# Kernel optimization log

Hardware: AMD Instinct MI355X
Metric: run time of the kernel (lower is better)

The kernel has to match this reference:

```python
import jax, jax.numpy as jnp
import numpy as np
from jax import lax

DN = ('NCHW', 'OIHW', 'NCHW')
SAME = ((1, 1), (1, 1))
VALID = ((0, 0), (0, 0))


def conv(x, w, pad):
    return lax.conv_general_dilated(x, w, (1, 1), pad, dimension_numbers=DN)


def convT(x, w, strides):
    # inverse (transposed) conv; for kernel==stride this exactly inverts the
    # non-overlapping pooling rulebook used by spconv's SparseInverseConv2d
    return lax.conv_transpose(x, w, strides, 'VALID', dimension_numbers=DN)


def maxpool(x, k):
    return lax.reduce_window(x, -jnp.inf, lax.max, (1, 1) + k, (1, 1) + k, 'VALID')


def lrelu(x):
    return jnp.where(x >= 0, x, 0.01 * x)  # F.leaky_relu default slope


def setup_inputs() -> dict:
    key = jax.random.key(0)
    ks = jax.random.split(key, 14)
    B, C, H, W = 32, 6, 500, 128
    x = jax.random.normal(ks[0], (B, C, H, W), jnp.float32)  # fully dense => all voxels active

    def p(k, shape):
        return jax.random.normal(k, shape, jnp.float32) * 0.05

    return {
        'x': x,
        'w1': p(ks[1], (8, 6, 3, 3)),      # SubMConv2d 6->8
        'w2': p(ks[2], (16, 8, 3, 3)),     # SubMConv2d 8->16
        'w3': p(ks[3], (32, 16, 3, 3)),    # SubMConv2d 16->32
        'wmu': p(ks[4], (1, 32, 1, 5)),    # SparseConv2d 32->1, kernel (1,5)
        'wlv': p(ks[5], (1, 32, 1, 5)),
        'wu0': p(ks[6], (32, 1, 1, 5)),    # SparseInverseConv2d 1->32
        'wu1': p(ks[7], (32, 32, 5, 2)),   # inverse of pool3
        'w4': p(ks[8], (16, 32, 3, 3)),
        'wu2': p(ks[9], (16, 16, 5, 2)),   # inverse of pool2
        'w5': p(ks[10], (8, 16, 3, 3)),
        'wu3': p(ks[11], (8, 8, 2, 2)),    # inverse of pool1
        'w6': p(ks[12], (6, 8, 3, 3)),
    }


def reference(x, w1, w2, w3, wmu, wlv, wu0, wu1, w4, wu2, w5, wu3, w6):
    B = x.shape[0]
    # ---- encoder ----
    h = lrelu(conv(x, w1, SAME))        # [B,8,500,128]
    h = maxpool(h, (2, 2))              # [B,8,250,64]
    h = lrelu(conv(h, w2, SAME))        # [B,16,250,64]
    h = maxpool(h, (5, 2))              # [B,16,50,32]
    h = lrelu(conv(h, w3, SAME))        # [B,32,50,32]
    h = maxpool(h, (5, 2))              # [B,32,10,16]
    mu = conv(h, wmu, VALID)            # [B,1,10,12]
    logvar = conv(h, wlv, VALID)        # [B,1,10,12]
    # ---- reparameterise ----
    eps = jax.random.normal(jax.random.key(42), mu.shape, mu.dtype)
    z = mu + eps * jnp.exp(0.5 * logvar)
    # ---- decoder ----
    d = lrelu(convT(z, wu0, (1, 1)))    # [B,32,10,16]
    d = lrelu(convT(d, wu1, (5, 2)))    # [B,32,50,32]
    d = lrelu(conv(d, w4, SAME))        # [B,16,50,32]
    d = lrelu(convT(d, wu2, (5, 2)))    # [B,16,250,64]
    d = lrelu(conv(d, w5, SAME))        # [B,8,250,64]
    d = lrelu(convT(d, wu3, (2, 2)))    # [B,8,500,128]
    d = lrelu(conv(d, w6, SAME))        # [B,6,500,128]
    return (d, mu.reshape(B, -1), logvar.reshape(B, -1), z.reshape(B, -1))
```

## Files before the change

kernel.cpp:

```cpp
#include <hip/hip_runtime.h>
#include <stdint.h>

#define DI __device__ __forceinline__

DI float lrelu(float x){ return x >= 0.0f ? x : 0.01f*x; }

DI uint32_t rotl32(uint32_t x, int d){ return (x << d) | (x >> (32 - d)); }

DI void threefry_0_42(uint32_t& x0, uint32_t& x1){
  const uint32_t ks0 = 0u, ks1 = 42u, ks2 = 0x1BD11BF0u;
  x0 += ks0; x1 += ks1;
  #define TFR(d) { x0 += x1; x1 = rotl32(x1,(d)); x1 ^= x0; }
  TFR(13) TFR(15) TFR(26) TFR(6)  x0 += ks1; x1 += ks2 + 1u;
  TFR(17) TFR(29) TFR(16) TFR(24) x0 += ks2; x1 += ks0 + 2u;
  TFR(13) TFR(15) TFR(26) TFR(6)  x0 += ks0; x1 += ks1 + 3u;
  TFR(17) TFR(29) TFR(16) TFR(24) x0 += ks1; x1 += ks2 + 4u;
  TFR(13) TFR(15) TFR(26) TFR(6)  x0 += ks2; x1 += ks0 + 5u;
  #undef TFR
}

DI float erfinv_f32(float x){
  float w = -log1pf(-x*x);
  float p;
  if (w < 5.0f){
    w = w - 2.5f;
    p = 2.81022636e-08f;
    p = fmaf(p, w, 3.43273939e-07f);
    p = fmaf(p, w, -3.5233877e-06f);
    p = fmaf(p, w, -4.39150654e-06f);
    p = fmaf(p, w, 0.00021858087f);
    p = fmaf(p, w, -0.00125372503f);
    p = fmaf(p, w, -0.00417768164f);
    p = fmaf(p, w, 0.246640727f);
    p = fmaf(p, w, 1.50140941f);
  } else {
    w = sqrtf(w) - 3.0f;
    p = -0.000200214257f;
    p = fmaf(p, w, 0.000100950558f);
    p = fmaf(p, w, 0.00134934322f);
    p = fmaf(p, w, -0.00367342844f);
    p = fmaf(p, w, 0.00573950773f);
    p = fmaf(p, w, -0.0076224613f);
    p = fmaf(p, w, 0.00943887047f);
    p = fmaf(p, w, 1.00167406f);
    p = fmaf(p, w, 2.83297682f);
  }
  return p * x;
}

#define OUT_D_OFF   0
#define OUT_MU_OFF  12288000
#define OUT_LV_OFF  (12288000 + 3840)
#define OUT_Z_OFF   (12288000 + 7680)

__global__ __launch_bounds__(256) void k_enc1(const float* __restrict__ x,
                                              const float* __restrict__ w1,
                                              float* __restrict__ p1){
  __shared__ float wl[432];
  int tid = threadIdx.x;
  for (int i = tid; i < 432; i += 256) wl[i] = w1[i];
  __syncthreads();
  int t = blockIdx.x*256 + tid;
  int pw = t & 63; int u = t >> 6; int ph = u % 250; int b = u / 250;
  float acc[2][2][8];
  #pragma unroll
  for (int a=0;a<2;a++)
    #pragma unroll
    for (int d=0;d<2;d++)
      #pragma unroll
      for (int o=0;o<8;o++) acc[a][d][o] = 0.0f;
  int r0 = 2*ph - 1, c0 = 2*pw - 1;
  #pragma unroll 2
  for (int c = 0; c < 6; ++c){
    float win[4][4];
    #pragma unroll
    for (int i=0;i<4;i++){
      int r = r0 + i; bool rok = ((unsigned)r < 500u);
      #pragma unroll
      for (int j=0;j<4;j++){
        int cc = c0 + j;
        win[i][j] = (rok && (unsigned)cc < 128u) ? x[((b*6+c)*500+r)*128+cc] : 0.0f;
      }
    }
    #pragma unroll
    for (int kh=0;kh<3;kh++)
      #pragma unroll
      for (int kw=0;kw<3;kw++){
        float wv[8];
        #pragma unroll
        for (int o=0;o<8;o++) wv[o] = wl[((o*6+c)*3+kh)*3+kw];
        #pragma unroll
        for (int dy=0;dy<2;dy++)
          #pragma unroll
          for (int dx=0;dx<2;dx++){
            float v = win[dy+kh][dx+kw];
            #pragma unroll
            for (int o=0;o<8;o++) acc[dy][dx][o] = fmaf(v, wv[o], acc[dy][dx][o]);
          }
      }
  }
  #pragma unroll
  for (int o=0;o<8;o++){
    float m = fmaxf(fmaxf(acc[0][0][o], acc[0][1][o]), fmaxf(acc[1][0][o], acc[1][1][o]));
    p1[((b*8+o)*250+ph)*64+pw] = lrelu(m);
  }
}

__global__ __launch_bounds__(256) void k_enc2(const float* __restrict__ in,
                                              const float* __restrict__ w2,
                                              float* __restrict__ p2){
  __shared__ float wl[1152];
  int tid = threadIdx.x;
  for (int i = tid; i < 1152; i += 256) wl[i] = w2[i];
  __syncthreads();
  int t = blockIdx.x*256 + tid;
  int dx = t & 1; int u = t >> 1;
  int pw = u & 31; u >>= 5; int ph = u % 50; int b = u / 50;
  int cw = 2*pw + dx;
  float acc[5][16];
  #pragma unroll
  for (int dy=0;dy<5;dy++)
    #pragma unroll
    for (int o=0;o<16;o++) acc[dy][o] = 0.0f;
  int r0 = 5*ph - 1, c0 = cw - 1;
  #pragma unroll 2
  for (int c = 0; c < 8; ++c){
    float win[7][3];
    #pragma unroll
    for (int i=0;i<7;i++){
      int r = r0 + i; bool rok = ((unsigned)r < 250u);
      #pragma unroll
      for (int j=0;j<3;j++){
        int cc = c0 + j;
        win[i][j] = (rok && (unsigned)cc < 64u) ? in[((b*8+c)*250+r)*64+cc] : 0.0f;
      }
    }
    #pragma unroll
    for (int kh=0;kh<3;kh++)
      #pragma unroll
      for (int kw=0;kw<3;kw++){
        float wv[16];
        #pragma unroll
        for (int o=0;o<16;o++) wv[o] = wl[((o*8+c)*3+kh)*3+kw];
        #pragma unroll
        for (int dy=0;dy<5;dy++){
          float v = win[dy+kh][kw];
          #pragma unroll
          for (int o=0;o<16;o++) acc[dy][o] = fmaf(v, wv[o], acc[dy][o]);
        }
      }
  }
  #pragma unroll
  for (int o=0;o<16;o++){
    float m = acc[0][o];
    #pragma unroll
    for (int dy=1;dy<5;dy++) m = fmaxf(m, acc[dy][o]);
    m = fmaxf(m, __shfl_xor(m, 1));
    if (dx == 0) p2[((b*16+o)*50+ph)*32+pw] = lrelu(m);
  }
}

__global__ __launch_bounds__(256) void k_conv3(const float* __restrict__ in,
                                               const float* __restrict__ w3,
                                               float* __restrict__ outp){
  __shared__ float wl[4608];
  int tid = threadIdx.x;
  for (int i = tid; i < 4608; i += 256) wl[i] = w3[i];
  __syncthreads();
  int t = blockIdx.x*256 + tid;
  int w = t & 31; int u = t >> 5; int h = u % 50; u /= 50; int oh = u & 1; int b = u >> 1;
  float acc[16];
  #pragma unroll
  for (int o=0;o<16;o++) acc[o] = 0.0f;
  int r0 = h - 1, c0 = w - 1;
  #pragma unroll 2
  for (int c = 0; c < 16; ++c){
    float win[3][3];
    #pragma unroll
    for (int i=0;i<3;i++){
      int r = r0 + i; bool rok = ((unsigned)r < 50u);
      #pragma unroll
      for (int j=0;j<3;j++){
        int cc = c0 + j;
        win[i][j] = (rok && (unsigned)cc < 32u) ? in[((b*16+c)*50+r)*32+cc] : 0.0f;
      }
    }
    #pragma unroll
    for (int kh=0;kh<3;kh++)
      #pragma unroll
      for (int kw=0;kw<3;kw++){
        float v = win[kh][kw];
        #pragma unroll
        for (int o=0;o<16;o++)
          acc[o] = fmaf(v, wl[(((oh*16+o)*16+c)*3+kh)*3+kw], acc[o]);
      }
  }
  #pragma unroll
  for (int o=0;o<16;o++)
    outp[((b*32 + oh*16 + o)*50 + h)*32 + w] = lrelu(acc[o]);
}

__global__ __launch_bounds__(256) void k_pool3(const float* __restrict__ in,
                                               float* __restrict__ outp){
  int t = blockIdx.x*256 + threadIdx.x;
  int pw = t & 15; int u = t >> 4; int ph = u % 10; u /= 10; int o = u & 31; int b = u >> 5;
  float m = -INFINITY;
  #pragma unroll
  for (int dh=0;dh<5;dh++)
    #pragma unroll
    for (int dw=0;dw<2;dw++)
      m = fmaxf(m, in[((b*32+o)*50 + 5*ph+dh)*32 + 2*pw+dw]);
  outp[((b*32+o)*10+ph)*16+pw] = m;
}

__global__ __launch_bounds__(256) void k_latent(const float* __restrict__ p3,
                                                const float* __restrict__ wmu,
                                                const float* __restrict__ wlv,
                                                float* __restrict__ outp){
  int t = blockIdx.x*256 + threadIdx.x;
  int w = t % 12; int h = (t/12) % 10; int b = t/120;
  float mu = 0.0f, lv = 0.0f;
  for (int c = 0; c < 32; ++c){
    const float* row = p3 + ((b*32+c)*10+h)*16 + w;
    #pragma unroll
    for (int kw=0;kw<5;kw++){
      float v = row[kw];
      mu = fmaf(v, wmu[c*5+kw], mu);
      lv = fmaf(v, wlv[c*5+kw], lv);
    }
  }
  uint32_t x0 = 0u, x1 = (uint32_t)t;
  threefry_0_42(x0, x1);
  uint32_t bits = x0 ^ x1;
  float f = __uint_as_float((bits >> 9) | 0x3f800000u) - 1.0f;
  const float lo = -0.99999994f;
  float uu = fmaxf(lo, f * 2.0f + lo);
  float eps = 1.41421356f * erfinv_f32(uu);
  float z = mu + eps * expf(0.5f * lv);
  outp[OUT_MU_OFF + t] = mu;
  outp[OUT_LV_OFF + t] = lv;
  outp[OUT_Z_OFF  + t] = z;
}

__global__ __launch_bounds__(256) void k_dec0(const float* __restrict__ outp,
                                              const float* __restrict__ wu0,
                                              float* __restrict__ d0){
  int t = blockIdx.x*256 + threadIdx.x;
  int w = t & 15; int u = t >> 4; int h = u % 10; u /= 10; int o = u & 31; int b = u >> 5;
  const float* z = outp + OUT_Z_OFF;
  float a = 0.0f;
  #pragma unroll
  for (int kw=0;kw<5;kw++){
    int ww = w + kw - 4;
    if ((unsigned)ww < 12u) a = fmaf(z[b*120 + h*12 + ww], wu0[o*5+kw], a);
  }
  d0[((b*32+o)*10+h)*16+w] = lrelu(a);
}

__global__ __launch_bounds__(256) void k_dec1(const float* __restrict__ d0,
                                              const float* __restrict__ wu1,
                                              float* __restrict__ d1){
  int t = blockIdx.x*256 + threadIdx.x;
  int wo = t & 31; int u = t >> 5; int ho = u % 50; u /= 50; int o = u & 31; int b = u >> 5;
  int i = ho / 5, r = ho - 5*i, jj = wo >> 1, s = wo & 1;
  const float* ip = d0 + b*5120 + i*16 + jj;
  const float* wp = wu1 + (o*32*5 + (4-r))*2 + (1-s);
  float a = 0.0f;
  #pragma unroll 8
  for (int c=0;c<32;c++) a = fmaf(ip[c*160], wp[c*10], a);
  d1[((b*32+o)*50+ho)*32+wo] = lrelu(a);
}

__global__ __launch_bounds__(256) void k_c4(const float* __restrict__ in,
                                            const float* __restrict__ w4,
                                            float* __restrict__ outp){
  __shared__ float wl[4608];
  int tid = threadIdx.x;
  for (int i = tid; i < 4608; i += 256) wl[i] = w4[i];
  __syncthreads();
  int t = blockIdx.x*256 + tid;
  int w = t & 31; int u = t >> 5; int h = u % 50; u /= 50; int oh = u & 1; int b = u >> 1;
  float acc[8];
  #pragma unroll
  for (int o=0;o<8;o++) acc[o] = 0.0f;
  int r0 = h - 1, c0 = w - 1;
  #pragma unroll 2
  for (int c = 0; c < 32; ++c){
    float win[3][3];
    #pragma unroll
    for (int i=0;i<3;i++){
      int r = r0 + i; bool rok = ((unsigned)r < 50u);
      #pragma unroll
      for (int j=0;j<3;j++){
        int cc = c0 + j;
        win[i][j] = (rok && (unsigned)cc < 32u) ? in[((b*32+c)*50+r)*32+cc] : 0.0f;
      }
    }
    #pragma unroll
    for (int kh=0;kh<3;kh++)
      #pragma unroll
      for (int kw=0;kw<3;kw++){
        float v = win[kh][kw];
        #pragma unroll
        for (int o=0;o<8;o++)
          acc[o] = fmaf(v, wl[(((oh*8+o)*32+c)*3+kh)*3+kw], acc[o]);
      }
  }
  #pragma unroll
  for (int o=0;o<8;o++)
    outp[((b*16 + oh*8 + o)*50 + h)*32 + w] = lrelu(acc[o]);
}

__global__ __launch_bounds__(256) void k_u2(const float* __restrict__ d2,
                                            const float* __restrict__ wu2,
                                            float* __restrict__ d3){
  int t = blockIdx.x*256 + threadIdx.x;
  int w = t & 63; int u = t >> 6; int h = u % 250; u /= 250; int o = u & 15; int b = u >> 4;
  int i = h / 5, r = h - 5*i, jj = w >> 1, s = w & 1;
  const float* ip = d2 + b*25600 + i*32 + jj;
  const float* wp = wu2 + (o*16*5 + (4-r))*2 + (1-s);
  float a = 0.0f;
  #pragma unroll 8
  for (int c=0;c<16;c++) a = fmaf(ip[c*1600], wp[c*10], a);
  d3[((b*16+o)*250+h)*64+w] = lrelu(a);
}

__global__ __launch_bounds__(256) void k_c5(const float* __restrict__ in,
                                            const float* __restrict__ w5,
                                            float* __restrict__ outp){
  __shared__ float wl[1152];
  int tid = threadIdx.x;
  for (int i = tid; i < 1152; i += 256) wl[i] = w5[i];
  __syncthreads();
  int t = blockIdx.x*256 + tid;
  int w = t & 63; int u = t >> 6; int h = u % 250; int b = u / 250;
  float acc[8];
  #pragma unroll
  for (int o=0;o<8;o++) acc[o] = 0.0f;
  int r0 = h - 1, c0 = w - 1;
  #pragma unroll 2
  for (int c = 0; c < 16; ++c){
    float win[3][3];
    #pragma unroll
    for (int i=0;i<3;i++){
      int r = r0 + i; bool rok = ((unsigned)r < 250u);
      #pragma unroll
      for (int j=0;j<3;j++){
        int cc = c0 + j;
        win[i][j] = (rok && (unsigned)cc < 64u) ? in[((b*16+c)*250+r)*64+cc] : 0.0f;
      }
    }
    #pragma unroll
    for (int kh=0;kh<3;kh++)
      #pragma unroll
      for (int kw=0;kw<3;kw++){
        float v = win[kh][kw];
        #pragma unroll
        for (int o=0;o<8;o++)
          acc[o] = fmaf(v, wl[((o*16+c)*3+kh)*3+kw], acc[o]);
      }
  }
  #pragma unroll
  for (int o=0;o<8;o++)
    outp[((b*8+o)*250+h)*64+w] = lrelu(acc[o]);
}

__global__ __launch_bounds__(256) void k_u3(const float* __restrict__ d4,
                                            const float* __restrict__ wu3,
                                            float* __restrict__ d5){
  int t = blockIdx.x*256 + threadIdx.x;
  int w = t & 127; int u = t >> 7; int h = u % 500; u /= 500; int o = u & 7; int b = u >> 3;
  int i = h >> 1, r = h & 1, jj = w >> 1, s = w & 1;
  const float* ip = d4 + b*128000 + i*64 + jj;
  const float* wp = wu3 + (o*8*2 + (1-r))*2 + (1-s);
  float a = 0.0f;
  #pragma unroll
  for (int c=0;c<8;c++) a = fmaf(ip[c*16000], wp[c*4], a);
  d5[((b*8+o)*500+h)*128+w] = lrelu(a);
}

__global__ __launch_bounds__(256) void k_c6(const float* __restrict__ in,
                                            const float* __restrict__ w6,
                                            float* __restrict__ outp){
  __shared__ float wl[432];
  int tid = threadIdx.x;
  for (int i = tid; i < 432; i += 256) wl[i] = w6[i];
  __syncthreads();
  int t = blockIdx.x*256 + tid;
  int w = t & 127; int u = t >> 7; int h = u % 500; int b = u / 500;
  float acc[6];
  #pragma unroll
  for (int o=0;o<6;o++) acc[o] = 0.0f;
  int r0 = h - 1, c0 = w - 1;
  #pragma unroll 2
  for (int c = 0; c < 8; ++c){
    float win[3][3];
    #pragma unroll
    for (int i=0;i<3;i++){
      int r = r0 + i; bool rok = ((unsigned)r < 500u);
      #pragma unroll
      for (int j=0;j<3;j++){
        int cc = c0 + j;
        win[i][j] = (rok && (unsigned)cc < 128u) ? in[((b*8+c)*500+r)*128+cc] : 0.0f;
      }
    }
    #pragma unroll
    for (int kh=0;kh<3;kh++)
      #pragma unroll
      for (int kw=0;kw<3;kw++){
        float v = win[kh][kw];
        #pragma unroll
        for (int o=0;o<6;o++)
          acc[o] = fmaf(v, wl[((o*8+c)*3+kh)*3+kw], acc[o]);
      }
  }
  #pragma unroll
  for (int o=0;o<6;o++)
    outp[((b*6+o)*500+h)*128+w] = lrelu(acc[o]);
}

extern "C" void kernel_launch(void* const* d_in, const int* in_sizes, int n_in,
                              void* d_out, int out_size, void* d_ws, size_t ws_size,
                              hipStream_t stream){
  const float* x   = (const float*)d_in[0];
  const float* w1  = (const float*)d_in[1];
  const float* w2  = (const float*)d_in[2];
  const float* w3  = (const float*)d_in[3];
  const float* wmu = (const float*)d_in[4];
  const float* wlv = (const float*)d_in[5];
  const float* wu0 = (const float*)d_in[6];
  const float* wu1 = (const float*)d_in[7];
  const float* w4  = (const float*)d_in[8];
  const float* wu2 = (const float*)d_in[9];
  const float* w5  = (const float*)d_in[10];
  const float* wu3 = (const float*)d_in[11];
  const float* w6  = (const float*)d_in[12];
  float* out = (float*)d_out;
  float* A  = (float*)d_ws;
  float* Bb = A + 4096000;

  k_enc1 <<<2000, 256, 0, stream>>>(x,  w1,  A);
  k_enc2 <<< 400, 256, 0, stream>>>(A,  w2,  Bb);
  k_conv3<<< 400, 256, 0, stream>>>(Bb, w3,  A);
  k_pool3<<< 640, 256, 0, stream>>>(A,  Bb);
  k_latent<<< 15, 256, 0, stream>>>(Bb, wmu, wlv, out);
  k_dec0 <<< 640, 256, 0, stream>>>(out, wu0, A);
  k_dec1 <<<6400, 256, 0, stream>>>(A,  wu1, Bb);
  k_c4   <<< 400, 256, 0, stream>>>(Bb, w4,  A);
  k_u2   <<<32000,256, 0, stream>>>(A,  wu2, Bb);
  k_c5   <<<2000, 256, 0, stream>>>(Bb, w5,  A);
  k_u3   <<<64000,256, 0, stream>>>(A,  wu3, Bb);
  k_c6   <<<2000, 256, 0, stream>>>(Bb, w6,  out);
}
```

Baseline: 414.4 us.

## Stage input halo tiles in shared memory for all 3x3 conv kernels

Each 3x3 conv kernel (enc1, enc2, conv3, c4, c5, c6) now loads a row band of the input, with a one-pixel halo for every channel, into shared memory. The grid is remapped to batch x row-band blocks, so overlapping window reads come from LDS instead of repeated global loads with bounds checks. Weights move out of shared memory and are read directly from global memory through uniform indices, which the compiler may turn into scalar loads. This adds a sync, padded edge work and larger LDS use that may lower occupancy, and c6 now runs with many more, smaller blocks.

```diff
diff --git a/kernel.cpp b/kernel.cpp
--- a/kernel.cpp
+++ b/kernel.cpp
@@ -56,12 +56,25 @@
 __global__ __launch_bounds__(256) void k_enc1(const float* __restrict__ x,
                                               const float* __restrict__ w1,
                                               float* __restrict__ p1){
-  __shared__ float wl[432];
+  __shared__ float tile[6*10*130];
   int tid = threadIdx.x;
-  for (int i = tid; i < 432; i += 256) wl[i] = w1[i];
+  int band = blockIdx.x % 63;
+  int b    = blockIdx.x / 63;
+  int r0 = band*8;
+  for (int idx = tid; idx < 6*10*130; idx += 256){
+    int lc = idx % 130;
+    int rest = idx / 130;
+    int lr = rest % 10;
+    int ch = rest / 10;
+    int gr = r0 - 1 + lr, gc = lc - 1;
+    float v = 0.0f;
+    if ((unsigned)gr < 500u && (unsigned)gc < 128u)
+      v = x[((b*6+ch)*500+gr)*128+gc];
+    tile[idx] = v;
+  }
   __syncthreads();
-  int t = blockIdx.x*256 + tid;
-  int pw = t & 63; int u = t >> 6; int ph = u % 250; int b = u / 250;
+  int pw = tid & 63, pr = tid >> 6;
+  int ph = band*4 + pr;
   float acc[2][2][8];
   #pragma unroll
   for (int a=0;a<2;a++)
@@ -69,26 +82,22 @@
     for (int d=0;d<2;d++)
       #pragma unroll
       for (int o=0;o<8;o++) acc[a][d][o] = 0.0f;
-  int r0 = 2*ph - 1, c0 = 2*pw - 1;
+  int base = (2*pr)*130 + 2*pw;
   #pragma unroll 2
   for (int c = 0; c < 6; ++c){
     float win[4][4];
     #pragma unroll
-    for (int i=0;i<4;i++){
-      int r = r0 + i; bool rok = ((unsigned)r < 500u);
-      #pragma unroll
-      for (int j=0;j<4;j++){
-        int cc = c0 + j;
-        win[i][j] = (rok && (unsigned)cc < 128u) ? x[((b*6+c)*500+r)*128+cc] : 0.0f;
-      }
-    }
+    for (int i=0;i<4;i++)
+      #pragma unroll
+      for (int j=0;j<4;j++)
+        win[i][j] = tile[c*1300 + base + i*130 + j];
     #pragma unroll
     for (int kh=0;kh<3;kh++)
       #pragma unroll
       for (int kw=0;kw<3;kw++){
         float wv[8];
         #pragma unroll
-        for (int o=0;o<8;o++) wv[o] = wl[((o*6+c)*3+kh)*3+kw];
+        for (int o=0;o<8;o++) wv[o] = w1[((o*6+c)*3+kh)*3+kw];
         #pragma unroll
         for (int dy=0;dy<2;dy++)
           #pragma unroll
@@ -99,49 +108,60 @@
           }
       }
   }
-  #pragma unroll
-  for (int o=0;o<8;o++){
-    float m = fmaxf(fmaxf(acc[0][0][o], acc[0][1][o]), fmaxf(acc[1][0][o], acc[1][1][o]));
-    p1[((b*8+o)*250+ph)*64+pw] = lrelu(m);
+  if (ph < 250){
+    #pragma unroll
+    for (int o=0;o<8;o++){
+      float m = fmaxf(fmaxf(acc[0][0][o], acc[0][1][o]), fmaxf(acc[1][0][o], acc[1][1][o]));
+      p1[((b*8+o)*250+ph)*64+pw] = lrelu(m);
+    }
   }
 }
 
 __global__ __launch_bounds__(256) void k_enc2(const float* __restrict__ in,
                                               const float* __restrict__ w2,
                                               float* __restrict__ p2){
-  __shared__ float wl[1152];
+  __shared__ float tile[8*22*66];
   int tid = threadIdx.x;
-  for (int i = tid; i < 1152; i += 256) wl[i] = w2[i];
+  int band = blockIdx.x % 13;
+  int b    = blockIdx.x / 13;
+  int r0 = band*20;
+  for (int idx = tid; idx < 8*22*66; idx += 256){
+    int lc = idx % 66;
+    int rest = idx / 66;
+    int lr = rest % 22;
+    int ch = rest / 22;
+    int gr = r0 - 1 + lr, gc = lc - 1;
+    float v = 0.0f;
+    if ((unsigned)gr < 250u && (unsigned)gc < 64u)
+      v = in[((b*8+ch)*250+gr)*64+gc];
+    tile[idx] = v;
+  }
   __syncthreads();
-  int t = blockIdx.x*256 + tid;
-  int dx = t & 1; int u = t >> 1;
-  int pw = u & 31; u >>= 5; int ph = u % 50; int b = u / 50;
+  int dx = tid & 1; int u = tid >> 1;
+  int pw = u & 31; int pr = (u >> 5) & 3;
   int cw = 2*pw + dx;
+  int ph = band*4 + pr;
   float acc[5][16];
   #pragma unroll
   for (int dy=0;dy<5;dy++)
     #pragma unroll
     for (int o=0;o<16;o++) acc[dy][o] = 0.0f;
-  int r0 = 5*ph - 1, c0 = cw - 1;
-  #pragma unroll 2
+  int base = (5*pr)*66 + cw;
+  #pragma unroll 1
   for (int c = 0; c < 8; ++c){
     float win[7][3];
     #pragma unroll
-    for (int i=0;i<7;i++){
-      int r = r0 + i; bool rok = ((unsigned)r < 250u);
-      #pragma unroll
-      for (int j=0;j<3;j++){
-        int cc = c0 + j;
-        win[i][j] = (rok && (unsigned)cc < 64u) ? in[((b*8+c)*250+r)*64+cc] : 0.0f;
-      }
-    }
+    for (int i=0;i<7;i++)
+      #pragma unroll
+      for (int j=0;j<3;j++)
+        win[i][j] = tile[c*1452 + base + i*66 + j];
     #pragma unroll
     for (int kh=0;kh<3;kh++)
       #pragma unroll
       for (int kw=0;kw<3;kw++){
         float wv[16];
         #pragma unroll
-        for (int o=0;o<16;o++) wv[o] = wl[((o*8+c)*3+kh)*3+kw];
+        for (int o=0;o<16;o++) wv[o] = w2[((o*8+c)*3+kh)*3+kw];
         #pragma unroll
         for (int dy=0;dy<5;dy++){
           float v = win[dy+kh][kw];
@@ -156,35 +176,44 @@
     #pragma unroll
     for (int dy=1;dy<5;dy++) m = fmaxf(m, acc[dy][o]);
     m = fmaxf(m, __shfl_xor(m, 1));
-    if (dx == 0) p2[((b*16+o)*50+ph)*32+pw] = lrelu(m);
+    if (dx == 0 && ph < 50) p2[((b*16+o)*50+ph)*32+pw] = lrelu(m);
   }
 }
 
 __global__ __launch_bounds__(256) void k_conv3(const float* __restrict__ in,
                                                const float* __restrict__ w3,
                                                float* __restrict__ outp){
-  __shared__ float wl[4608];
+  __shared__ float tile[16*10*34];
   int tid = threadIdx.x;
-  for (int i = tid; i < 4608; i += 256) wl[i] = w3[i];
+  int bi = blockIdx.x;
+  int band = bi % 7; int oh = (bi/7) & 1; int b = bi / 14;
+  int r0 = band*8;
+  for (int idx = tid; idx < 16*10*34; idx += 256){
+    int lc = idx % 34;
+    int rest = idx / 34;
+    int lr = rest % 10;
+    int ch = rest / 10;
+    int gr = r0 - 1 + lr, gc = lc - 1;
+    float v = 0.0f;
+    if ((unsigned)gr < 50u && (unsigned)gc < 32u)
+      v = in[((b*16+ch)*50+gr)*32+gc];
+    tile[idx] = v;
+  }
   __syncthreads();
-  int t = blockIdx.x*256 + tid;
-  int w = t & 31; int u = t >> 5; int h = u % 50; u /= 50; int oh = u & 1; int b = u >> 1;
+  int col = tid & 31, tr = tid >> 5;
+  int h = r0 + tr;
   float acc[16];
   #pragma unroll
   for (int o=0;o<16;o++) acc[o] = 0.0f;
-  int r0 = h - 1, c0 = w - 1;
+  int base = tr*34 + col;
   #pragma unroll 2
   for (int c = 0; c < 16; ++c){
     float win[3][3];
     #pragma unroll
-    for (int i=0;i<3;i++){
-      int r = r0 + i; bool rok = ((unsigned)r < 50u);
-      #pragma unroll
-      for (int j=0;j<3;j++){
-        int cc = c0 + j;
-        win[i][j] = (rok && (unsigned)cc < 32u) ? in[((b*16+c)*50+r)*32+cc] : 0.0f;
-      }
-    }
+    for (int i=0;i<3;i++)
+      #pragma unroll
+      for (int j=0;j<3;j++)
+        win[i][j] = tile[c*340 + base + i*34 + j];
     #pragma unroll
     for (int kh=0;kh<3;kh++)
       #pragma unroll
@@ -192,12 +221,14 @@
         float v = win[kh][kw];
         #pragma unroll
         for (int o=0;o<16;o++)
-          acc[o] = fmaf(v, wl[(((oh*16+o)*16+c)*3+kh)*3+kw], acc[o]);
+          acc[o] = fmaf(v, w3[(((oh*16+o)*16+c)*3+kh)*3+kw], acc[o]);
       }
   }
-  #pragma unroll
-  for (int o=0;o<16;o++)
-    outp[((b*32 + oh*16 + o)*50 + h)*32 + w] = lrelu(acc[o]);
+  if (h < 50){
+    #pragma unroll
+    for (int o=0;o<16;o++)
+      outp[((b*32 + oh*16 + o)*50 + h)*32 + col] = lrelu(acc[o]);
+  }
 }
 
 __global__ __launch_bounds__(256) void k_pool3(const float* __restrict__ in,
@@ -274,28 +305,37 @@
 __global__ __launch_bounds__(256) void k_c4(const float* __restrict__ in,
                                             const float* __restrict__ w4,
                                             float* __restrict__ outp){
-  __shared__ float wl[4608];
+  __shared__ float tile[32*10*34];
   int tid = threadIdx.x;
-  for (int i = tid; i < 4608; i += 256) wl[i] = w4[i];
+  int bi = blockIdx.x;
+  int band = bi % 7; int oh = (bi/7) & 1; int b = bi / 14;
+  int r0 = band*8;
+  for (int idx = tid; idx < 32*10*34; idx += 256){
+    int lc = idx % 34;
+    int rest = idx / 34;
+    int lr = rest % 10;
+    int ch = rest / 10;
+    int gr = r0 - 1 + lr, gc = lc - 1;
+    float v = 0.0f;
+    if ((unsigned)gr < 50u && (unsigned)gc < 32u)
+      v = in[((b*32+ch)*50+gr)*32+gc];
+    tile[idx] = v;
+  }
   __syncthreads();
-  int t = blockIdx.x*256 + tid;
-  int w = t & 31; int u = t >> 5; int h = u % 50; u /= 50; int oh = u & 1; int b = u >> 1;
+  int col = tid & 31, tr = tid >> 5;
+  int h = r0 + tr;
   float acc[8];
   #pragma unroll
   for (int o=0;o<8;o++) acc[o] = 0.0f;
-  int r0 = h - 1, c0 = w - 1;
+  int base = tr*34 + col;
   #pragma unroll 2
   for (int c = 0; c < 32; ++c){
     float win[3][3];
     #pragma unroll
-    for (int i=0;i<3;i++){
-      int r = r0 + i; bool rok = ((unsigned)r < 50u);
-      #pragma unroll
-      for (int j=0;j<3;j++){
-        int cc = c0 + j;
-        win[i][j] = (rok && (unsigned)cc < 32u) ? in[((b*32+c)*50+r)*32+cc] : 0.0f;
-      }
-    }
+    for (int i=0;i<3;i++)
+      #pragma unroll
+      for (int j=0;j<3;j++)
+        win[i][j] = tile[c*340 + base + i*34 + j];
     #pragma unroll
     for (int kh=0;kh<3;kh++)
       #pragma unroll
@@ -303,12 +343,14 @@
         float v = win[kh][kw];
         #pragma unroll
         for (int o=0;o<8;o++)
-          acc[o] = fmaf(v, wl[(((oh*8+o)*32+c)*3+kh)*3+kw], acc[o]);
+          acc[o] = fmaf(v, w4[(((oh*8+o)*32+c)*3+kh)*3+kw], acc[o]);
       }
   }
-  #pragma unroll
-  for (int o=0;o<8;o++)
-    outp[((b*16 + oh*8 + o)*50 + h)*32 + w] = lrelu(acc[o]);
+  if (h < 50){
+    #pragma unroll
+    for (int o=0;o<8;o++)
+      outp[((b*16 + oh*8 + o)*50 + h)*32 + col] = lrelu(acc[o]);
+  }
 }
 
 __global__ __launch_bounds__(256) void k_u2(const float* __restrict__ d2,
@@ -328,28 +370,37 @@
 __global__ __launch_bounds__(256) void k_c5(const float* __restrict__ in,
                                             const float* __restrict__ w5,
                                             float* __restrict__ outp){
-  __shared__ float wl[1152];
+  __shared__ float tile[16*6*66];
   int tid = threadIdx.x;
-  for (int i = tid; i < 1152; i += 256) wl[i] = w5[i];
+  int band = blockIdx.x % 63;
+  int b    = blockIdx.x / 63;
+  int r0 = band*4;
+  for (int idx = tid; idx < 16*6*66; idx += 256){
+    int lc = idx % 66;
+    int rest = idx / 66;
+    int lr = rest % 6;
+    int ch = rest / 6;
+    int gr = r0 - 1 + lr, gc = lc - 1;
+    float v = 0.0f;
+    if ((unsigned)gr < 250u && (unsigned)gc < 64u)
+      v = in[((b*16+ch)*250+gr)*64+gc];
+    tile[idx] = v;
+  }
   __syncthreads();
-  int t = blockIdx.x*256 + tid;
-  int w = t & 63; int u = t >> 6; int h = u % 250; int b = u / 250;
+  int col = tid & 63, tr = tid >> 6;
+  int h = r0 + tr;
   float acc[8];
   #pragma unroll
   for (int o=0;o<8;o++) acc[o] = 0.0f;
-  int r0 = h - 1, c0 = w - 1;
+  int base = tr*66 + col;
   #pragma unroll 2
   for (int c = 0; c < 16; ++c){
     float win[3][3];
     #pragma unroll
-    for (int i=0;i<3;i++){
-      int r = r0 + i; bool rok = ((unsigned)r < 250u);
-      #pragma unroll
-      for (int j=0;j<3;j++){
-        int cc = c0 + j;
-        win[i][j] = (rok && (unsigned)cc < 64u) ? in[((b*16+c)*250+r)*64+cc] : 0.0f;
-      }
-    }
+    for (int i=0;i<3;i++)
+      #pragma unroll
+      for (int j=0;j<3;j++)
+        win[i][j] = tile[c*396 + base + i*66 + j];
     #pragma unroll
     for (int kh=0;kh<3;kh++)
       #pragma unroll
@@ -357,12 +408,14 @@
         float v = win[kh][kw];
         #pragma unroll
         for (int o=0;o<8;o++)
-          acc[o] = fmaf(v, wl[((o*16+c)*3+kh)*3+kw], acc[o]);
+          acc[o] = fmaf(v, w5[((o*16+c)*3+kh)*3+kw], acc[o]);
       }
   }
-  #pragma unroll
-  for (int o=0;o<8;o++)
-    outp[((b*8+o)*250+h)*64+w] = lrelu(acc[o]);
+  if (h < 250){
+    #pragma unroll
+    for (int o=0;o<8;o++)
+      outp[((b*8+o)*250+h)*64+col] = lrelu(acc[o]);
+  }
 }
 
 __global__ __launch_bounds__(256) void k_u3(const float* __restrict__ d4,
@@ -382,28 +435,37 @@
 __global__ __launch_bounds__(256) void k_c6(const float* __restrict__ in,
                                             const float* __restrict__ w6,
                                             float* __restrict__ outp){
-  __shared__ float wl[432];
+  __shared__ float tile[8*4*130];
   int tid = threadIdx.x;
-  for (int i = tid; i < 432; i += 256) wl[i] = w6[i];
+  int band = blockIdx.x % 250;
+  int b    = blockIdx.x / 250;
+  int r0 = band*2;
+  for (int idx = tid; idx < 8*4*130; idx += 256){
+    int lc = idx % 130;
+    int rest = idx / 130;
+    int lr = rest & 3;
+    int ch = rest >> 2;
+    int gr = r0 - 1 + lr, gc = lc - 1;
+    float v = 0.0f;
+    if ((unsigned)gr < 500u && (unsigned)gc < 128u)
+      v = in[((b*8+ch)*500+gr)*128+gc];
+    tile[idx] = v;
+  }
   __syncthreads();
-  int t = blockIdx.x*256 + tid;
-  int w = t & 127; int u = t >> 7; int h = u % 500; int b = u / 500;
+  int col = tid & 127, tr = tid >> 7;
+  int h = r0 + tr;
   float acc[6];
   #pragma unroll
   for (int o=0;o<6;o++) acc[o] = 0.0f;
-  int r0 = h - 1, c0 = w - 1;
+  int base = tr*130 + col;
   #pragma unroll 2
   for (int c = 0; c < 8; ++c){
     float win[3][3];
     #pragma unroll
-    for (int i=0;i<3;i++){
-      int r = r0 + i; bool rok = ((unsigned)r < 500u);
-      #pragma unroll
-      for (int j=0;j<3;j++){
-        int cc = c0 + j;
-        win[i][j] = (rok && (unsigned)cc < 128u) ? in[((b*8+c)*500+r)*128+cc] : 0.0f;
-      }
-    }
+    for (int i=0;i<3;i++)
+      #pragma unroll
+      for (int j=0;j<3;j++)
+        win[i][j] = tile[c*520 + base + i*130 + j];
     #pragma unroll
     for (int kh=0;kh<3;kh++)
       #pragma unroll
@@ -411,12 +473,12 @@
         float v = win[kh][kw];
         #pragma unroll
         for (int o=0;o<6;o++)
-          acc[o] = fmaf(v, wl[((o*8+c)*3+kh)*3+kw], acc[o]);
+          acc[o] = fmaf(v, w6[((o*8+c)*3+kh)*3+kw], acc[o]);
       }
   }
   #pragma unroll
   for (int o=0;o<6;o++)
-    outp[((b*6+o)*500+h)*128+w] = lrelu(acc[o]);
+    outp[((b*6+o)*500+h)*128+col] = lrelu(acc[o]);
 }
 
 extern "C" void kernel_launch(void* const* d_in, const int* in_sizes, int n_in,
@@ -439,16 +501,16 @@
   float* A  = (float*)d_ws;
   float* Bb = A + 4096000;
 
-  k_enc1 <<<2000, 256, 0, stream>>>(x,  w1,  A);
-  k_enc2 <<< 400, 256, 0, stream>>>(A,  w2,  Bb);
-  k_conv3<<< 400, 256, 0, stream>>>(Bb, w3,  A);
+  k_enc1 <<<2016, 256, 0, stream>>>(x,  w1,  A);
+  k_enc2 <<< 416, 256, 0, stream>>>(A,  w2,  Bb);
+  k_conv3<<< 448, 256, 0, stream>>>(Bb, w3,  A);
   k_pool3<<< 640, 256, 0, stream>>>(A,  Bb);
   k_latent<<< 15, 256, 0, stream>>>(Bb, wmu, wlv, out);
   k_dec0 <<< 640, 256, 0, stream>>>(out, wu0, A);
   k_dec1 <<<6400, 256, 0, stream>>>(A,  wu1, Bb);
-  k_c4   <<< 400, 256, 0, stream>>>(Bb, w4,  A);
+  k_c4   <<< 448, 256, 0, stream>>>(Bb, w4,  A);
   k_u2   <<<32000,256, 0, stream>>>(A,  wu2, Bb);
-  k_c5   <<<2000, 256, 0, stream>>>(Bb, w5,  A);
+  k_c5   <<<2016, 256, 0, stream>>>(Bb, w5,  A);
   k_u3   <<<64000,256, 0, stream>>>(A,  wu3, Bb);
-  k_c6   <<<2000, 256, 0, stream>>>(Bb, w6,  out);
-}
+  k_c6   <<<8000, 256, 0, stream>>>(Bb, w6,  out);
+}
```

New measurement: 454.5 us. 1.1x slower.
